# Kernel optimization log

Hardware: AMD Instinct MI355X
Metric: run time of the kernel (lower is better)

## Reference

```python
import jax, jax.numpy as jnp
import numpy as np

TAU = 0.2
EPS = 1e-12  # matches torch F.normalize eps


def _l2_normalize(x):
    # F.normalize(x, p=2, dim=1): x / max(||x||, eps)
    norm = jnp.sqrt(jnp.sum(x * x, axis=1, keepdims=True))
    return x / jnp.maximum(norm, EPS)


def setup_inputs() -> dict:
    key = jax.random.key(0)
    k1, k2 = jax.random.split(key)
    N, D = 16384, 256
    z1 = jax.random.normal(k1, (N, D), dtype=jnp.float32)
    z2 = jax.random.normal(k2, (N, D), dtype=jnp.float32)
    return {"z1": z1, "z2": z2}


def reference(z1, z2):
    # semi_loss: f(x) = exp(x / tau) over full cosine-similarity matrix
    h1 = _l2_normalize(z1)
    h2 = _l2_normalize(z2)
    sim = jnp.einsum('nd,md->nm', h1, h2)          # [N, N] cosine similarities
    between = jnp.exp(sim / TAU)                   # f(pair_sim)
    diag = jnp.diagonal(between)                   # positive pairs
    row_sum = jnp.sum(between, axis=1)
    loss = jnp.sum(-jnp.log(diag / (row_sum - diag)))
    return loss
```

## Files before the change

### kernel.cpp

```cpp
#include <hip/hip_runtime.h>
#include <hip/hip_bf16.h>

#define NROWS 16384
#define DDIM  256
#define LOG2E 1.4426950408889634f
#define SCALE 7.213475204444817f

typedef __attribute__((ext_vector_type(4))) float f32x4;
typedef __attribute__((ext_vector_type(2))) float f32x2;
typedef __attribute__((ext_vector_type(4))) int   i32x4;
typedef __attribute__((ext_vector_type(8))) int   i32x8;

#define UNIT_SCALE 0x7F7F7F7F

__global__ __launch_bounds__(256) void prep_kernel(
    const float* __restrict__ z1, const float* __restrict__ z2,
    unsigned char* __restrict__ h1q, unsigned char* __restrict__ h2q,
    float* __restrict__ diag5, float* __restrict__ rowsum) {
  int tid = threadIdx.x;
  int w = tid >> 6, lane = tid & 63;
  int r = blockIdx.x * 4 + w;

  const float4 a = ((const float4*)z1)[r * 64 + lane];
  const float4 b = ((const float4*)z2)[r * 64 + lane];

  float ss1 = a.x * a.x + a.y * a.y + a.z * a.z + a.w * a.w;
  float ss2 = b.x * b.x + b.y * b.y + b.z * b.z + b.w * b.w;
  float dp  = a.x * b.x + a.y * b.y + a.z * b.z + a.w * b.w;
  #pragma unroll
  for (int m = 1; m <= 32; m <<= 1) {
    ss1 += __shfl_xor(ss1, m);
    ss2 += __shfl_xor(ss2, m);
    dp  += __shfl_xor(dp, m);
  }
  float inv1 = 1.0f / fmaxf(sqrtf(ss1), 1e-12f);
  float inv2 = 1.0f / fmaxf(sqrtf(ss2), 1e-12f);
  float s1 = inv1 * SCALE;

  int p1 = __builtin_amdgcn_cvt_pk_fp8_f32(a.x * s1, a.y * s1, 0, false);
  p1     = __builtin_amdgcn_cvt_pk_fp8_f32(a.z * s1, a.w * s1, p1, true);
  int p2 = __builtin_amdgcn_cvt_pk_fp8_f32(b.x * inv2, b.y * inv2, 0, false);
  p2     = __builtin_amdgcn_cvt_pk_fp8_f32(b.z * inv2, b.w * inv2, p2, true);
  ((int*)h1q)[r * 64 + lane] = p1;
  ((int*)h2q)[r * 64 + lane] = p2;

  if (lane == 0) diag5[r] = dp * inv1 * inv2 * 5.0f;
  if (tid < 4) rowsum[blockIdx.x * 4 + tid] = 0.0f;
}

#define CSPL 16
#define BN   64
#define NJT  ((NROWS / CSPL) / BN)

__global__ __launch_bounds__(256) void simexp_kernel(
    const unsigned char* __restrict__ h1q, const unsigned char* __restrict__ h2q,
    float* __restrict__ rowsum) {
  __shared__ alignas(16) unsigned char lds[2][BN * DDIM];

  int tid = threadIdx.x, w = tid >> 6, lane = tid & 63;
  int bx = blockIdx.x;
  int rb = bx >> 4;
  int cs = bx & 15;
  int row0 = rb * 256 + w * 64;
  int c0 = cs * (NROWS / CSPL);

  const char* h1b = (const char*)h1q;
  const char* h2b = (const char*)h2q;

  i32x8 afr[4][2];
  #pragma unroll
  for (int m = 0; m < 4; ++m)
    #pragma unroll
    for (int ks = 0; ks < 2; ++ks) {
      int row = row0 + m * 16 + (lane & 15);
      int off = row * 256 + ks * 128 + (lane >> 4) * 32;
      afr[m][ks] = *reinterpret_cast<const i32x8*>(h1b + off);
    }
  #pragma unroll
  for (int m = 0; m < 4; ++m)
    #pragma unroll
    for (int ks = 0; ks < 2; ++ks)
      asm volatile("" : "+v"(afr[m][ks]));

  int sw  = (lane & 7) << 4;
  int pA  = (lane & 15) * 256 + (((lane >> 4) * 32) ^ sw);
  int pB  = (lane & 15) * 256 + ((((lane >> 4) * 32) + 16) ^ sw);

  int kb = (lane & 15) * 16;
  const char* P[4];
  #pragma unroll
  for (int i = 0; i < 4; ++i) {
    int rit = w * 16 + i * 4 + (lane >> 4);
    P[i] = h2b + (size_t)(c0 + rit) * 256 + (kb ^ ((rit & 7) << 4));
  }

  f32x2 rs2[4][2];
  #pragma unroll
  for (int m = 0; m < 4; ++m) {
    rs2[m][0] = (f32x2){0.f, 0.f};
    rs2[m][1] = (f32x2){0.f, 0.f};
  }

  auto stage = [&](int buf) {
    #pragma unroll
    for (int i = 0; i < 4; ++i) {
      __builtin_amdgcn_global_load_lds(
          (const __attribute__((address_space(1))) void*)P[i],
          (__attribute__((address_space(3))) void*)&lds[buf][w * 4096 + i * 1024],
          16, 0, 0);
      P[i] += 16384;
    }
  };

  stage(0);
  __syncthreads();

  for (int jt = 0; jt < NJT; ++jt) {
    int cur = jt & 1;
    if (jt + 1 < NJT) stage(cur ^ 1);

    const char* L = (const char*)&lds[cur][0];
    #pragma unroll
    for (int n = 0; n < 4; ++n) {
      f32x4 acc[4];
      #pragma unroll
      for (int m = 0; m < 4; ++m) acc[m] = (f32x4){0.f, 0.f, 0.f, 0.f};

      #pragma unroll
      for (int ks = 0; ks < 2; ++ks) {
        i32x4 lo = *reinterpret_cast<const i32x4*>(L + pA + (n * 4096 + ks * 128));
        i32x4 hi = *reinterpret_cast<const i32x4*>(L + pB + (n * 4096 + ks * 128));
        union { i32x8 v; i32x4 h[2]; } u;
        u.h[0] = lo; u.h[1] = hi;
        #pragma unroll
        for (int m = 0; m < 4; ++m)
          acc[m] = __builtin_amdgcn_mfma_scale_f32_16x16x128_f8f6f4(
              afr[m][ks], u.v, acc[m],
              0 , 0 ,
              0, UNIT_SCALE, 0, UNIT_SCALE);
      }
      #pragma unroll
      for (int m = 0; m < 4; ++m) {
        rs2[m][0] += (f32x2){__builtin_amdgcn_exp2f(acc[m][0]),
                             __builtin_amdgcn_exp2f(acc[m][1])};
        rs2[m][1] += (f32x2){__builtin_amdgcn_exp2f(acc[m][2]),
                             __builtin_amdgcn_exp2f(acc[m][3])};
      }
    }
    __syncthreads();
  }

  #pragma unroll
  for (int m = 0; m < 4; ++m)
    #pragma unroll
    for (int p = 0; p < 2; ++p)
      #pragma unroll
      for (int c = 0; c < 2; ++c) {
        float v = rs2[m][p][c];
        v += __shfl_xor(v, 1);
        v += __shfl_xor(v, 2);
        v += __shfl_xor(v, 4);
        v += __shfl_xor(v, 8);
        if ((lane & 15) == 0)
          atomicAdd(&rowsum[row0 + m * 16 + (lane >> 4) * 4 + p * 2 + c], v);
      }
}

__global__ __launch_bounds__(1024) void loss_kernel(
    const float* __restrict__ rowsum, const float* __restrict__ diag5,
    float* __restrict__ out) {
  int tid = threadIdx.x;
  float s = 0.0f;
  for (int i = tid; i < NROWS; i += 1024) {
    float d5 = diag5[i];
    float de = __builtin_amdgcn_exp2f(d5 * LOG2E);
    s += logf(rowsum[i] - de) - d5;
  }
  #pragma unroll
  for (int m = 1; m <= 32; m <<= 1) s += __shfl_xor(s, m);
  __shared__ float wsum[16];
  if ((tid & 63) == 0) wsum[tid >> 6] = s;
  __syncthreads();
  if (tid == 0) {
    float t = 0.0f;
    #pragma unroll
    for (int i = 0; i < 16; ++i) t += wsum[i];
    out[0] = t;
  }
}

extern "C" void kernel_launch(void* const* d_in, const int* in_sizes, int n_in,
                              void* d_out, int out_size, void* d_ws, size_t ws_size,
                              hipStream_t stream) {
  const float* z1 = (const float*)d_in[0];
  const float* z2 = (const float*)d_in[1];

  char* ws = (char*)d_ws;
  unsigned char* h1q = (unsigned char*)(ws);
  unsigned char* h2q = (unsigned char*)(ws + 4194304);
  float* diag5 = (float*)(ws + 8388608);
  float* rowsm = (float*)(ws + 8454144);
  if (ws_size < 8519680) return;

  prep_kernel<<<4096, 256, 0, stream>>>(z1, z2, h1q, h2q, diag5, rowsm);
  simexp_kernel<<<1024, 256, 0, stream>>>(h1q, h2q, rowsm);
  loss_kernel<<<1, 1024, 0, stream>>>(rowsm, diag5, (float*)d_out);
}
```

Before: 88.32 us.

## Software-pipeline MFMA and exp across column tiles and halve column splits

The simexp kernel now uses two ping-pong accumulator sets, so the exp2 and row-sum work for one 16-column sub-tile is interleaved with the MFMAs of the next one, and the last tile's exp is finished after the loop. The column split drops from 16 to 8, so 512 blocks each sweep twice as many column tiles. This reduces the number of atomics and of A-fragment reloads per block. In exchange there are fewer blocks to fill the CUs (512 on 256 CUs) and higher register pressure from the extra accumulators.

```diff
diff --git a/kernel.cpp b/kernel.cpp
--- a/kernel.cpp
+++ b/kernel.cpp
@@ -48,9 +48,31 @@
   if (tid < 4) rowsum[blockIdx.x * 4 + tid] = 0.0f;
 }
 
-#define CSPL 16
+#define CSPL 8
 #define BN   64
 #define NJT  ((NROWS / CSPL) / BN)
+
+#define ZACC(A) do { _Pragma("unroll") \
+  for (int m = 0; m < 4; ++m) A[m] = (f32x4){0.f, 0.f, 0.f, 0.f}; } while (0)
+
+#define DO_MFMA(NN, A) do { _Pragma("unroll") \
+  for (int ks = 0; ks < 2; ++ks) { \
+    i32x4 lo = *reinterpret_cast<const i32x4*>(L + pA + (NN * 4096 + ks * 128)); \
+    i32x4 hi = *reinterpret_cast<const i32x4*>(L + pB + (NN * 4096 + ks * 128)); \
+    union { i32x8 v; i32x4 h[2]; } u; u.h[0] = lo; u.h[1] = hi; \
+    _Pragma("unroll") \
+    for (int m = 0; m < 4; ++m) \
+      A[m] = __builtin_amdgcn_mfma_scale_f32_16x16x128_f8f6f4( \
+          afr[m][ks], u.v, A[m], 0, 0, 0, UNIT_SCALE, 0, UNIT_SCALE); \
+  } } while (0)
+
+#define DO_EXP(A) do { _Pragma("unroll") \
+  for (int m = 0; m < 4; ++m) { \
+    rs2[m][0] += (f32x2){__builtin_amdgcn_exp2f(A[m][0]), \
+                         __builtin_amdgcn_exp2f(A[m][1])}; \
+    rs2[m][1] += (f32x2){__builtin_amdgcn_exp2f(A[m][2]), \
+                         __builtin_amdgcn_exp2f(A[m][3])}; \
+  } } while (0)
 
 __global__ __launch_bounds__(256) void simexp_kernel(
     const unsigned char* __restrict__ h1q, const unsigned char* __restrict__ h2q,
@@ -59,8 +81,8 @@
 
   int tid = threadIdx.x, w = tid >> 6, lane = tid & 63;
   int bx = blockIdx.x;
-  int rb = bx >> 4;
-  int cs = bx & 15;
+  int rb = bx >> 3;
+  int cs = bx & 7;
   int row0 = rb * 256 + w * 64;
   int c0 = cs * (NROWS / CSPL);
 
@@ -87,11 +109,16 @@
   int pB  = (lane & 15) * 256 + ((((lane >> 4) * 32) + 16) ^ sw);
 
   int kb = (lane & 15) * 16;
-  const char* P[4];
-  #pragma unroll
-  for (int i = 0; i < 4; ++i) {
-    int rit = w * 16 + i * 4 + (lane >> 4);
-    P[i] = h2b + (size_t)(c0 + rit) * 256 + (kb ^ ((rit & 7) << 4));
+  const char* P0; const char* P1; const char* P2; const char* P3;
+  {
+    int r0_ = w * 16 + 0 * 4 + (lane >> 4);
+    int r1_ = w * 16 + 1 * 4 + (lane >> 4);
+    int r2_ = w * 16 + 2 * 4 + (lane >> 4);
+    int r3_ = w * 16 + 3 * 4 + (lane >> 4);
+    P0 = h2b + (size_t)(c0 + r0_) * 256 + (kb ^ ((r0_ & 7) << 4));
+    P1 = h2b + (size_t)(c0 + r1_) * 256 + (kb ^ ((r1_ & 7) << 4));
+    P2 = h2b + (size_t)(c0 + r2_) * 256 + (kb ^ ((r2_ & 7) << 4));
+    P3 = h2b + (size_t)(c0 + r3_) * 256 + (kb ^ ((r3_ & 7) << 4));
   }
 
   f32x2 rs2[4][2];
@@ -102,53 +129,48 @@
   }
 
   auto stage = [&](int buf) {
-    #pragma unroll
-    for (int i = 0; i < 4; ++i) {
-      __builtin_amdgcn_global_load_lds(
-          (const __attribute__((address_space(1))) void*)P[i],
-          (__attribute__((address_space(3))) void*)&lds[buf][w * 4096 + i * 1024],
-          16, 0, 0);
-      P[i] += 16384;
-    }
+    __builtin_amdgcn_global_load_lds(
+        (const __attribute__((address_space(1))) void*)P0,
+        (__attribute__((address_space(3))) void*)&lds[buf][w * 4096 + 0 * 1024], 16, 0, 0);
+    __builtin_amdgcn_global_load_lds(
+        (const __attribute__((address_space(1))) void*)P1,
+        (__attribute__((address_space(3))) void*)&lds[buf][w * 4096 + 1 * 1024], 16, 0, 0);
+    __builtin_amdgcn_global_load_lds(
+        (const __attribute__((address_space(1))) void*)P2,
+        (__attribute__((address_space(3))) void*)&lds[buf][w * 4096 + 2 * 1024], 16, 0, 0);
+    __builtin_amdgcn_global_load_lds(
+        (const __attribute__((address_space(1))) void*)P3,
+        (__attribute__((address_space(3))) void*)&lds[buf][w * 4096 + 3 * 1024], 16, 0, 0);
+    P0 += 16384; P1 += 16384; P2 += 16384; P3 += 16384;
   };
 
   stage(0);
   __syncthreads();
+
+  f32x4 accA[4], accB[4];
 
   for (int jt = 0; jt < NJT; ++jt) {
     int cur = jt & 1;
     if (jt + 1 < NJT) stage(cur ^ 1);
 
     const char* L = (const char*)&lds[cur][0];
-    #pragma unroll
-    for (int n = 0; n < 4; ++n) {
-      f32x4 acc[4];
-      #pragma unroll
-      for (int m = 0; m < 4; ++m) acc[m] = (f32x4){0.f, 0.f, 0.f, 0.f};
-
-      #pragma unroll
-      for (int ks = 0; ks < 2; ++ks) {
-        i32x4 lo = *reinterpret_cast<const i32x4*>(L + pA + (n * 4096 + ks * 128));
-        i32x4 hi = *reinterpret_cast<const i32x4*>(L + pB + (n * 4096 + ks * 128));
-        union { i32x8 v; i32x4 h[2]; } u;
-        u.h[0] = lo; u.h[1] = hi;
-        #pragma unroll
-        for (int m = 0; m < 4; ++m)
-          acc[m] = __builtin_amdgcn_mfma_scale_f32_16x16x128_f8f6f4(
-              afr[m][ks], u.v, acc[m],
-              0 , 0 ,
-              0, UNIT_SCALE, 0, UNIT_SCALE);
-      }
-      #pragma unroll
-      for (int m = 0; m < 4; ++m) {
-        rs2[m][0] += (f32x2){__builtin_amdgcn_exp2f(acc[m][0]),
-                             __builtin_amdgcn_exp2f(acc[m][1])};
-        rs2[m][1] += (f32x2){__builtin_amdgcn_exp2f(acc[m][2]),
-                             __builtin_amdgcn_exp2f(acc[m][3])};
-      }
-    }
+
+    ZACC(accA);
+    DO_MFMA(0, accA);
+    if (jt) DO_EXP(accB);
+    ZACC(accB);
+    DO_MFMA(1, accB);
+    DO_EXP(accA);
+    ZACC(accA);
+    DO_MFMA(2, accA);
+    DO_EXP(accB);
+    ZACC(accB);
+    DO_MFMA(3, accB);
+    DO_EXP(accA);
+
     __syncthreads();
   }
+  DO_EXP(accB);
 
   #pragma unroll
   for (int m = 0; m < 4; ++m)
@@ -203,6 +225,6 @@
   if (ws_size < 8519680) return;
 
   prep_kernel<<<4096, 256, 0, stream>>>(z1, z2, h1q, h2q, diag5, rowsm);
-  simexp_kernel<<<1024, 256, 0, stream>>>(h1q, h2q, rowsm);
+  simexp_kernel<<<512, 256, 0, stream>>>(h1q, h2q, rowsm);
   loss_kernel<<<1, 1024, 0, stream>>>(rowsm, diag5, (float*)d_out);
 }
```

Result: slower. 90.15 us (+2.1%).

## Pre-tile B operand in fragment order and load directly to registers, bypassing LDS

Applied to the files above, without the earlier changes.

The prep kernel now writes the normalized FP8 z2 matrix in a tiled layout that matches the MFMA B-fragment order. The similarity kernel can then load B straight from global memory into registers with coalesced 16-byte loads, double-buffered across two register sets, and drops LDS staging and the per-tile __syncthreads. The column split is halved, so there are fewer blocks, each doing more columns. The aim is to remove LDS traffic and barrier overhead, at the cost of higher register pressure and reliance on L2 hit rate for the B data that all warps share.

```diff
diff --git a/kernel.cpp b/kernel.cpp
--- a/kernel.cpp
+++ b/kernel.cpp
@@ -15,7 +15,7 @@
 
 __global__ __launch_bounds__(256) void prep_kernel(
     const float* __restrict__ z1, const float* __restrict__ z2,
-    unsigned char* __restrict__ h1q, unsigned char* __restrict__ h2q,
+    unsigned char* __restrict__ h1q, unsigned char* __restrict__ h2t,
     float* __restrict__ diag5, float* __restrict__ rowsum) {
   int tid = threadIdx.x;
   int w = tid >> 6, lane = tid & 63;
@@ -42,30 +42,61 @@
   int p2 = __builtin_amdgcn_cvt_pk_fp8_f32(b.x * inv2, b.y * inv2, 0, false);
   p2     = __builtin_amdgcn_cvt_pk_fp8_f32(b.z * inv2, b.w * inv2, p2, true);
   ((int*)h1q)[r * 64 + lane] = p1;
-  ((int*)h2q)[r * 64 + lane] = p2;
+
+  {
+    int c = lane >> 2, sub = lane & 3;
+    int off = (r >> 4) * 4096 + (c >> 3) * 2048 + (c & 1) * 1024 +
+              ((c >> 1) & 3) * 256 + (r & 15) * 16 + sub * 4;
+    *(int*)(h2t + off) = p2;
+  }
 
   if (lane == 0) diag5[r] = dp * inv1 * inv2 * 5.0f;
   if (tid < 4) rowsum[blockIdx.x * 4 + tid] = 0.0f;
 }
 
-#define CSPL 16
-#define BN   64
-#define NJT  ((NROWS / CSPL) / BN)
+#define CSPL 8
+
+#define LOADSET(B, P0, P1) do { \
+  B[0] = *reinterpret_cast<const i32x4*>(P0); \
+  B[1] = *reinterpret_cast<const i32x4*>(P0 + 1024); \
+  B[2] = *reinterpret_cast<const i32x4*>(P0 + 2048); \
+  B[3] = *reinterpret_cast<const i32x4*>(P0 + 3072); \
+  B[4] = *reinterpret_cast<const i32x4*>(P1); \
+  B[5] = *reinterpret_cast<const i32x4*>(P1 + 1024); \
+  B[6] = *reinterpret_cast<const i32x4*>(P1 + 2048); \
+  B[7] = *reinterpret_cast<const i32x4*>(P1 + 3072); \
+  P0 += 8192; P1 += 8192; } while (0)
+
+#define MFMA_S(Aop, Bop, Cop) \
+  __builtin_amdgcn_mfma_scale_f32_16x16x128_f8f6f4( \
+      Aop, Bop, Cop, 0, 0, 0, UNIT_SCALE, 0, UNIT_SCALE)
+
+#define COMPUTE(B) do { \
+  union { i32x8 v; i32x4 h[2]; } u00, u01, u10, u11; \
+  u00.h[0] = B[0]; u00.h[1] = B[1]; u01.h[0] = B[2]; u01.h[1] = B[3]; \
+  u10.h[0] = B[4]; u10.h[1] = B[5]; u11.h[0] = B[6]; u11.h[1] = B[7]; \
+  f32x4 a0[4], a1[4]; \
+  _Pragma("unroll") for (int m = 0; m < 4; ++m) a0[m] = MFMA_S(afr[m][0], u00.v, ZV); \
+  _Pragma("unroll") for (int m = 0; m < 4; ++m) a1[m] = MFMA_S(afr[m][0], u10.v, ZV); \
+  _Pragma("unroll") for (int m = 0; m < 4; ++m) a0[m] = MFMA_S(afr[m][1], u01.v, a0[m]); \
+  _Pragma("unroll") for (int m = 0; m < 4; ++m) a1[m] = MFMA_S(afr[m][1], u11.v, a1[m]); \
+  _Pragma("unroll") for (int m = 0; m < 4; ++m) { \
+    rs2[m][0] += (f32x2){__builtin_amdgcn_exp2f(a0[m][0]), __builtin_amdgcn_exp2f(a0[m][1])}; \
+    rs2[m][1] += (f32x2){__builtin_amdgcn_exp2f(a0[m][2]), __builtin_amdgcn_exp2f(a0[m][3])}; \
+    rs2[m][0] += (f32x2){__builtin_amdgcn_exp2f(a1[m][0]), __builtin_amdgcn_exp2f(a1[m][1])}; \
+    rs2[m][1] += (f32x2){__builtin_amdgcn_exp2f(a1[m][2]), __builtin_amdgcn_exp2f(a1[m][3])}; \
+  } } while (0)
 
 __global__ __launch_bounds__(256) void simexp_kernel(
-    const unsigned char* __restrict__ h1q, const unsigned char* __restrict__ h2q,
+    const unsigned char* __restrict__ h1q, const unsigned char* __restrict__ h2t,
     float* __restrict__ rowsum) {
-  __shared__ alignas(16) unsigned char lds[2][BN * DDIM];
-
   int tid = threadIdx.x, w = tid >> 6, lane = tid & 63;
   int bx = blockIdx.x;
-  int rb = bx >> 4;
-  int cs = bx & 15;
+  int rb = bx >> 3;
+  int cs = bx & 7;
   int row0 = rb * 256 + w * 64;
-  int c0 = cs * (NROWS / CSPL);
 
   const char* h1b = (const char*)h1q;
-  const char* h2b = (const char*)h2q;
 
   i32x8 afr[4][2];
   #pragma unroll
@@ -82,18 +113,10 @@
     for (int ks = 0; ks < 2; ++ks)
       asm volatile("" : "+v"(afr[m][ks]));
 
-  int sw  = (lane & 7) << 4;
-  int pA  = (lane & 15) * 256 + (((lane >> 4) * 32) ^ sw);
-  int pB  = (lane & 15) * 256 + ((((lane >> 4) * 32) + 16) ^ sw);
+  const char* Bp0 = (const char*)h2t + (size_t)cs * 524288 + lane * 16;
+  const char* Bp1 = Bp0 + 4096;
 
-  int kb = (lane & 15) * 16;
-  const char* P[4];
-  #pragma unroll
-  for (int i = 0; i < 4; ++i) {
-    int rit = w * 16 + i * 4 + (lane >> 4);
-    P[i] = h2b + (size_t)(c0 + rit) * 256 + (kb ^ ((rit & 7) << 4));
-  }
-
+  const f32x4 ZV = {0.f, 0.f, 0.f, 0.f};
   f32x2 rs2[4][2];
   #pragma unroll
   for (int m = 0; m < 4; ++m) {
@@ -101,53 +124,14 @@
     rs2[m][1] = (f32x2){0.f, 0.f};
   }
 
-  auto stage = [&](int buf) {
-    #pragma unroll
-    for (int i = 0; i < 4; ++i) {
-      __builtin_amdgcn_global_load_lds(
-          (const __attribute__((address_space(1))) void*)P[i],
-          (__attribute__((address_space(3))) void*)&lds[buf][w * 4096 + i * 1024],
-          16, 0, 0);
-      P[i] += 16384;
-    }
-  };
+  i32x4 bufA[8], bufB[8];
+  LOADSET(bufA, Bp0, Bp1);
 
-  stage(0);
-  __syncthreads();
-
-  for (int jt = 0; jt < NJT; ++jt) {
-    int cur = jt & 1;
-    if (jt + 1 < NJT) stage(cur ^ 1);
-
-    const char* L = (const char*)&lds[cur][0];
-    #pragma unroll
-    for (int n = 0; n < 4; ++n) {
-      f32x4 acc[4];
-      #pragma unroll
-      for (int m = 0; m < 4; ++m) acc[m] = (f32x4){0.f, 0.f, 0.f, 0.f};
-
-      #pragma unroll
-      for (int ks = 0; ks < 2; ++ks) {
-        i32x4 lo = *reinterpret_cast<const i32x4*>(L + pA + (n * 4096 + ks * 128));
-        i32x4 hi = *reinterpret_cast<const i32x4*>(L + pB + (n * 4096 + ks * 128));
-        union { i32x8 v; i32x4 h[2]; } u;
-        u.h[0] = lo; u.h[1] = hi;
-        #pragma unroll
-        for (int m = 0; m < 4; ++m)
-          acc[m] = __builtin_amdgcn_mfma_scale_f32_16x16x128_f8f6f4(
-              afr[m][ks], u.v, acc[m],
-              0 , 0 ,
-              0, UNIT_SCALE, 0, UNIT_SCALE);
-      }
-      #pragma unroll
-      for (int m = 0; m < 4; ++m) {
-        rs2[m][0] += (f32x2){__builtin_amdgcn_exp2f(acc[m][0]),
-                             __builtin_amdgcn_exp2f(acc[m][1])};
-        rs2[m][1] += (f32x2){__builtin_amdgcn_exp2f(acc[m][2]),
-                             __builtin_amdgcn_exp2f(acc[m][3])};
-      }
-    }
-    __syncthreads();
+  for (int jt2 = 0; jt2 < 32; ++jt2) {
+    LOADSET(bufB, Bp0, Bp1);
+    COMPUTE(bufA);
+    LOADSET(bufA, Bp0, Bp1);
+    COMPUTE(bufB);
   }
 
   #pragma unroll
@@ -197,12 +181,12 @@
 
   char* ws = (char*)d_ws;
   unsigned char* h1q = (unsigned char*)(ws);
-  unsigned char* h2q = (unsigned char*)(ws + 4194304);
-  float* diag5 = (float*)(ws + 8388608);
-  float* rowsm = (float*)(ws + 8454144);
-  if (ws_size < 8519680) return;
+  unsigned char* h2t = (unsigned char*)(ws + 4194304);
+  float* diag5 = (float*)(ws + 8421376);
+  float* rowsm = (float*)(ws + 8486912);
+  if (ws_size < 8552448) return;
 
-  prep_kernel<<<4096, 256, 0, stream>>>(z1, z2, h1q, h2q, diag5, rowsm);
-  simexp_kernel<<<1024, 256, 0, stream>>>(h1q, h2q, rowsm);
+  prep_kernel<<<4096, 256, 0, stream>>>(z1, z2, h1q, h2t, diag5, rowsm);
+  simexp_kernel<<<512, 256, 0, stream>>>(h1q, h2t, rowsm);
   loss_kernel<<<1, 1024, 0, stream>>>(rowsm, diag5, (float*)d_out);
 }
```

Measured after the change: 88.37 us. About the same (+0.1%).
